# Kernel tuning notes

Hardware: AMD Instinct MI355X
Metric: run time of the kernel (lower is better)

## Reference

```python
import jax, jax.numpy as jnp
import numpy as np

LN_EPS = 1e-5
COS_EPS2 = 1e-16  # torch cosine_similarity: (n1*n2).clamp_min(eps**2), eps=1e-8


def _ln(x, g, b):
    m = jnp.mean(x, -1, keepdims=True)
    v = jnp.mean((x - m) ** 2, -1, keepdims=True)
    return (x - m) * jax.lax.rsqrt(v + LN_EPS) * g + b


def _span_pool(x, starts, ends, word_length):
    # x: [B, S, D] (text_feat[:, 1:]); spans pooled into slots 1..S of a [B, S+1, D] buffer
    B, S, D = x.shape
    cs = jnp.concatenate([jnp.zeros((B, 1, D), x.dtype), jnp.cumsum(x, axis=1)], axis=1)  # [B, S+1, D]
    pool = (jnp.take_along_axis(cs, ends[..., None], axis=1)
            - jnp.take_along_axis(cs, starts[..., None], axis=1))  # [B, S, D]
    mask = (jnp.arange(S)[None, :] < word_length[:, None]).astype(x.dtype)[..., None]
    return jnp.pad(pool * mask, ((0, 0), (1, 0), (0, 0)))  # [B, S+1, D], slot 0 = zeros


def _forward(text_hidden, vit_feature, pooler_out, target_mask, adj,
             ln_g, ln_b, wq, wk, wv, fc_w, mha_ln_g, mha_ln_b,
             w1a, b1a, w1b, b1b, w2a, b2a, w2b, b2b,
             loc_w, loc_b, out_w, out_b, word_length, tran_indices):
    B, L, D = text_hidden.shape
    H = wq.shape[1] // D  # n_head=4, d_k=d_v=768

    # eval mode: all dropouts are identity
    text_feat = _ln(text_hidden, ln_g, ln_b)

    # MultiHeadAttention(text_feat, vit, vit)
    q = (text_feat @ wq).reshape(B, L, H, D)
    k = (vit_feature @ wk).reshape(B, -1, H, D)
    v = (vit_feature @ wv).reshape(B, -1, H, D)
    attn = jnp.einsum('blhd,bmhd->bhlm', q, k) / jnp.sqrt(jnp.asarray(D, text_feat.dtype))
    attn = jax.nn.softmax(attn, axis=-1)
    ctx = jnp.einsum('bhlm,bmhd->blhd', attn, v).reshape(B, L, H * D)
    text_include_img = _ln(ctx @ fc_w + text_feat, mha_ln_g, mha_ln_b)

    # pairwise cosine similarity over sequence positions: [B, L, L]
    n = jnp.linalg.norm(text_include_img, axis=-1)
    sim = jnp.einsum('bld,bmd->blm', text_include_img, text_include_img)
    sim = sim / jnp.maximum(n[:, :, None] * n[:, None, :], COS_EPS2)

    global_bert = _ln(pooler_out, ln_g, ln_b)

    # span pooling of subword features into word slots (tmps buffers)
    starts, ends = tran_indices[..., 0], tran_indices[..., 1]
    tmps = _span_pool(text_feat[:, 1:, :], starts, ends, word_length)
    tmps_ti = _span_pool(text_include_img[:, 1:, :], starts, ends, word_length)

    adj_ti = adj * sim
    den = jnp.sum(adj, axis=2, keepdims=True) + 1.0
    den_ti = jnp.sum(adj_ti, axis=2, keepdims=True) + 1.0

    # NOTE: original loop recomputes from tmps each layer and only keeps the last
    # iteration, so only W1[-1]/W2[-1] affect the output (faithfully reproduced).
    g_dep = jax.nn.relu(((adj @ tmps) @ w1b + b1b) / den)
    g_ti = jax.nn.relu(((adj_ti @ tmps_ti) @ w2b + b2b) / den_ti)

    asp_wn = jnp.sum(target_mask, axis=1, keepdims=True)  # [B, 1]
    m = target_mask[:, :, None]
    gcn_out_text = jnp.sum(g_dep * m, axis=1) / asp_wn
    gcn_out_ti = jnp.sum(g_ti * m, axis=1) / asp_wn

    local_feat = jnp.concatenate([gcn_out_text, gcn_out_ti], axis=1) @ loc_w + loc_b
    feat = jnp.concatenate([global_bert, local_feat], axis=1)
    return feat @ out_w + out_b


def setup_inputs():
    key = jax.random.key(0)
    ks = jax.random.split(key, 20)
    B, L, NV, D, H, NC = 64, 160, 197, 768, 4, 3
    S = L - 1
    s = 0.02
    text_hidden = jax.random.normal(ks[0], (B, L, D), jnp.float32)
    vit_feature = jax.random.normal(ks[1], (B, NV, D), jnp.float32)
    pooler_out = jax.random.normal(ks[2], (B, D), jnp.float32)
    adj = jax.random.uniform(ks[3], (B, L, L), jnp.float32)
    target_mask = jnp.zeros((B, L), jnp.float32).at[:, 1:9].set(1.0)
    word_length = jax.random.randint(ks[4], (B,), 1, S, jnp.int32)
    lens = jax.random.randint(ks[5], (B, S), 1, 3, jnp.int32)  # 1-2 subtokens per word
    cum = jnp.cumsum(lens, axis=1)
    ends = jnp.minimum(cum, S)
    starts = jnp.minimum(cum - lens, S)
    tran_indices = jnp.stack([starts, ends], axis=-1).astype(jnp.int32)
    return dict(
        text_hidden=text_hidden, vit_feature=vit_feature, pooler_out=pooler_out,
        target_mask=target_mask, adj=adj,
        ln_g=jnp.ones((D,), jnp.float32), ln_b=jnp.zeros((D,), jnp.float32),
        wq=jax.random.normal(ks[6], (D, H * D), jnp.float32) * s,
        wk=jax.random.normal(ks[7], (D, H * D), jnp.float32) * s,
        wv=jax.random.normal(ks[8], (D, H * D), jnp.float32) * s,
        fc_w=jax.random.normal(ks[9], (H * D, D), jnp.float32) * s,
        mha_ln_g=jnp.ones((D,), jnp.float32), mha_ln_b=jnp.zeros((D,), jnp.float32),
        w1a=jax.random.normal(ks[10], (D, D), jnp.float32) * s, b1a=jnp.zeros((D,), jnp.float32),
        w1b=jax.random.normal(ks[11], (D, D), jnp.float32) * s, b1b=jnp.zeros((D,), jnp.float32),
        w2a=jax.random.normal(ks[12], (D, D), jnp.float32) * s, b2a=jnp.zeros((D,), jnp.float32),
        w2b=jax.random.normal(ks[13], (D, D), jnp.float32) * s, b2b=jnp.zeros((D,), jnp.float32),
        loc_w=jax.random.normal(ks[14], (2 * D, D), jnp.float32) * s, loc_b=jnp.zeros((D,), jnp.float32),
        out_w=jax.random.normal(ks[15], (2 * D, NC), jnp.float32) * s, out_b=jnp.zeros((NC,), jnp.float32),
        word_length=word_length, tran_indices=tran_indices,
    )


def reference(text_hidden, vit_feature, pooler_out, target_mask, adj,
              ln_g, ln_b, wq, wk, wv, fc_w, mha_ln_g, mha_ln_b,
              w1a, b1a, w1b, b1b, w2a, b2a, w2b, b2b,
              loc_w, loc_b, out_w, out_b, word_length, tran_indices):
    return _forward(text_hidden, vit_feature, pooler_out, target_mask, adj,
                    ln_g, ln_b, wq, wk, wv, fc_w, mha_ln_g, mha_ln_b,
                    w1a, b1a, w1b, b1b, w2a, b2a, w2b, b2b,
                    loc_w, loc_b, out_w, out_b, word_length, tran_indices)
```

## Files before the change

### kernel.cpp

```cpp
#include <hip/hip_runtime.h>
#include <math.h>

#define BB 64
#define LL 160
#define DD 768
#define HH 4
#define NVV 197
#define SS 159

typedef unsigned short u16;
typedef __attribute__((ext_vector_type(8))) short bf16x8;
typedef __attribute__((ext_vector_type(4))) float f32x4;

union QU { uint4 u; bf16x8 v; };

__device__ __forceinline__ u16 f2bf(float a) {
  unsigned u = __builtin_bit_cast(unsigned, a);
  u = (u + 0x7FFFu + ((u >> 16) & 1u)) >> 16;
  return (u16)u;
}
__device__ __forceinline__ unsigned f2bf2(float a, float b) {
  return (unsigned)f2bf(a) | ((unsigned)f2bf(b) << 16);
}
__device__ __forceinline__ float bf2f(u16 h) {
  unsigned u = ((unsigned)h) << 16;
  return __builtin_bit_cast(float, u);
}
__device__ __forceinline__ float to_f(float x) { return x; }
__device__ __forceinline__ float to_f(u16 x) { return bf2f(x); }

__device__ __forceinline__ void async16(const u16* g, void* l) {
  __builtin_amdgcn_global_load_lds(
      (const __attribute__((address_space(1))) void*)g,
      (__attribute__((address_space(3))) void*)l, 16, 0, 0);
}

__device__ __forceinline__ uint4 load_bf8(const u16* __restrict__ P, long long rowbase,
                                          int valid, int kb, int K) {
  uint4 r;
  if (valid && (kb + 8 <= K) && (((rowbase + kb) & 7) == 0)) {
    r = *(const uint4*)(P + rowbase + kb);
  } else {
    u16 e[8];
    #pragma unroll
    for (int i = 0; i < 8; ++i) { int k = kb + i; e[i] = (valid && k < K) ? P[rowbase + k] : (u16)0; }
    r.x = e[0] | ((unsigned)e[1] << 16); r.y = e[2] | ((unsigned)e[3] << 16);
    r.z = e[4] | ((unsigned)e[5] << 16); r.w = e[6] | ((unsigned)e[7] << 16);
  }
  return r;
}

__device__ __forceinline__ uint4 load_row8(const float* __restrict__ P, long long rowbase,
                                           int valid_row, int kb, int K) {
  float f[8];
  if (valid_row && (kb + 8 <= K)) {
    const float4* p0 = (const float4*)(P + rowbase + kb);
    float4 x = p0[0], y = p0[1];
    f[0] = x.x; f[1] = x.y; f[2] = x.z; f[3] = x.w;
    f[4] = y.x; f[5] = y.y; f[6] = y.z; f[7] = y.w;
  } else {
    #pragma unroll
    for (int e = 0; e < 8; ++e) { int k = kb + e; f[e] = (valid_row && k < K) ? P[rowbase + k] : 0.f; }
  }
  uint4 r;
  r.x = f2bf2(f[0], f[1]); r.y = f2bf2(f[2], f[3]);
  r.z = f2bf2(f[4], f[5]); r.w = f2bf2(f[6], f[7]);
  return r;
}

__device__ __forceinline__ uint4 load_a(const u16* P, long long rb, int v, int kb, int K) {
  return load_bf8(P, rb, v, kb, K);
}
__device__ __forceinline__ uint4 load_a(const float* P, long long rb, int v, int kb, int K) {
  return load_row8(P, rb, v, kb, K);
}

__global__ __launch_bounds__(256) void gemm2ph(
    const u16* __restrict__ A, const u16* __restrict__ Bm,
    float* __restrict__ Cf, u16* __restrict__ Cb,
    int M, int N, int K, int lda, int ldb, int ldc, int nbx,
    float alpha, const float* __restrict__ bias, const u16* __restrict__ residB,
    const float* __restrict__ rowdiv, int relu, int accum) {
  __shared__ uint4 As[4][128];
  __shared__ uint4 Bs[4][64];

  int nwg = gridDim.x;
  int id = blockIdx.x;
  int qq = nwg >> 3, rr = nwg & 7;
  int xcd = id & 7, idx = id >> 3;
  int swz = (xcd < rr ? xcd * (qq + 1) : rr * (qq + 1) + (xcd - rr) * qq) + idx;
  int bx = swz % nbx, by = swz / nbx;
  int row0 = by * 128, col0 = bx * 64;

  int t = threadIdx.x, l = t & 63, w = t >> 6;
  int wr = w * 32;
  int nt = K >> 5;

  int ra0 = row0 + l;       if (ra0 > M - 1) ra0 = M - 1;
  int ra1 = row0 + 64 + l;  if (ra1 > M - 1) ra1 = M - 1;
  int rb0 = col0 + l;       if (rb0 > N - 1) rb0 = N - 1;
  const u16* Ap0 = A + (long long)ra0 * lda + w * 8;
  const u16* Ap1 = A + (long long)ra1 * lda + w * 8;
  const u16* Bp0 = Bm + (long long)rb0 * ldb + w * 8;

  f32x4 acc[2][4] = {};

  for (int tt = 0; tt < nt; ++tt) {
    int kk = tt << 5;
    async16(Ap0 + kk, &As[w][0]);
    async16(Ap1 + kk, &As[w][64]);
    async16(Bp0 + kk, &Bs[w][0]);
    __syncthreads();
    int kg = l >> 4, li = l & 15;
    QU a[2], b[4];
    #pragma unroll
    for (int i = 0; i < 2; ++i) a[i].u = As[kg][wr + i * 16 + li];
    #pragma unroll
    for (int j = 0; j < 4; ++j) b[j].u = Bs[kg][j * 16 + li];
    #pragma unroll
    for (int i = 0; i < 2; ++i)
      #pragma unroll
      for (int j = 0; j < 4; ++j)
        acc[i][j] = __builtin_amdgcn_mfma_f32_16x16x32_bf16(a[i].v, b[j].v, acc[i][j], 0, 0, 0);
    __syncthreads();
  }

  #pragma unroll
  for (int i = 0; i < 2; ++i) {
    #pragma unroll
    for (int j = 0; j < 4; ++j) {
      int colj = col0 + j * 16 + (l & 15);
      float bv = (bias && colj < N) ? bias[colj] : 0.f;
      #pragma unroll
      for (int r = 0; r < 4; ++r) {
        int gr = row0 + wr + i * 16 + (l >> 4) * 4 + r;
        if (gr < M && colj < N) {
          long long ci = (long long)gr * ldc + colj;
          float v = acc[i][j][r] * alpha + bv;
          if (residB) v += bf2f(residB[ci]);
          if (accum) v += Cf[ci];
          if (rowdiv) v /= rowdiv[gr];
          if (relu) v = fmaxf(v, 0.f);
          if (Cf) Cf[ci] = v;
          if (Cb) Cb[ci] = f2bf(v);
        }
      }
    }
  }
}

template<bool TRANSB, typename TA>
__global__ __launch_bounds__(256) void gemm_bf16(
    const TA* __restrict__ A, const u16* __restrict__ Bm,
    float* __restrict__ Cf, u16* __restrict__ Cb,
    int M, int N, int K, int lda, int ldb, int ldc, int Hb,
    long long sAb, long long sAh, long long sBb, long long sBh,
    long long sCb, long long sCh,
    float alpha, const float* __restrict__ bias) {
  int bb = blockIdx.z / Hb, hh = blockIdx.z % Hb;
  A += bb * sAb + hh * sAh;
  Bm += bb * sBb + hh * sBh;
  long long coff = bb * sCb + hh * sCh;

  __shared__ uint4 As4[4][64];
  __shared__ uint4 Bs4[4][64];

  int row0 = blockIdx.y * 64, col0 = blockIdx.x * 64;
  int t = threadIdx.x;
  int l = t & 63, w = t >> 6;
  int mq = (w >> 1) * 32, nq = (w & 1) * 32;

  int am = t >> 2, akq = t & 3;
  int bn = t & 63, bkq = t >> 6;

  f32x4 acc[2][2] = {};

  for (int k0 = 0; k0 < K; k0 += 32) {
    As4[akq][am] = load_a(A, (long long)(row0 + am) * lda, (row0 + am) < M, k0 + akq * 8, K);
    if (TRANSB) {
      Bs4[akq][am] = load_bf8(Bm, (long long)(col0 + am) * ldb, (col0 + am) < N, k0 + akq * 8, K);
    } else {
      int gn = col0 + bn;
      u16 e[8];
      #pragma unroll
      for (int i = 0; i < 8; ++i) {
        int k = k0 + bkq * 8 + i;
        e[i] = (gn < N && k < K) ? Bm[(long long)k * ldb + gn] : (u16)0;
      }
      uint4 r;
      r.x = e[0] | ((unsigned)e[1] << 16); r.y = e[2] | ((unsigned)e[3] << 16);
      r.z = e[4] | ((unsigned)e[5] << 16); r.w = e[6] | ((unsigned)e[7] << 16);
      Bs4[bkq][bn] = r;
    }
    __syncthreads();
    int kg = l >> 4, li = l & 15;
    QU a0, a1, b0, b1;
    a0.u = As4[kg][mq + li];
    a1.u = As4[kg][mq + 16 + li];
    b0.u = Bs4[kg][nq + li];
    b1.u = Bs4[kg][nq + 16 + li];
    acc[0][0] = __builtin_amdgcn_mfma_f32_16x16x32_bf16(a0.v, b0.v, acc[0][0], 0, 0, 0);
    acc[0][1] = __builtin_amdgcn_mfma_f32_16x16x32_bf16(a0.v, b1.v, acc[0][1], 0, 0, 0);
    acc[1][0] = __builtin_amdgcn_mfma_f32_16x16x32_bf16(a1.v, b0.v, acc[1][0], 0, 0, 0);
    acc[1][1] = __builtin_amdgcn_mfma_f32_16x16x32_bf16(a1.v, b1.v, acc[1][1], 0, 0, 0);
    __syncthreads();
  }

  #pragma unroll
  for (int i = 0; i < 2; ++i) {
    #pragma unroll
    for (int j = 0; j < 2; ++j) {
      int colj = col0 + nq + j * 16 + (l & 15);
      float bv = (bias && colj < N) ? bias[colj] : 0.f;
      #pragma unroll
      for (int r = 0; r < 4; ++r) {
        int gr = row0 + mq + i * 16 + (l >> 4) * 4 + r;
        if (gr < M && colj < N) {
          long long ci = coff + (long long)gr * ldc + colj;
          float v = acc[i][j][r] * alpha + bv;
          if (Cf) Cf[ci] = v;
          if (Cb) Cb[ci] = f2bf(v);
        }
      }
    }
  }
}

__global__ __launch_bounds__(256) void sim_kernel(
    const float* __restrict__ TII, const float* __restrict__ nrm,
    const float* __restrict__ adjf, u16* __restrict__ adjtiB) {
  int bb = blockIdx.z;
  const float* T = TII + (long long)bb * LL * DD;

  __shared__ uint4 As4[4][64];
  __shared__ uint4 Bs4[4][64];

  int row0 = blockIdx.y * 64, col0 = blockIdx.x * 64;
  int t = threadIdx.x;
  int l = t & 63, w = t >> 6;
  int mq = (w >> 1) * 32, nq = (w & 1) * 32;
  int am = t >> 2, akq = t & 3;

  f32x4 acc[2][2] = {};

  for (int k0 = 0; k0 < DD; k0 += 32) {
    As4[akq][am] = load_row8(T, (long long)(row0 + am) * DD, (row0 + am) < LL, k0 + akq * 8, DD);
    Bs4[akq][am] = load_row8(T, (long long)(col0 + am) * DD, (col0 + am) < LL, k0 + akq * 8, DD);
    __syncthreads();
    int kg = l >> 4, li = l & 15;
    QU a0, a1, b0, b1;
    a0.u = As4[kg][mq + li];
    a1.u = As4[kg][mq + 16 + li];
    b0.u = Bs4[kg][nq + li];
    b1.u = Bs4[kg][nq + 16 + li];
    acc[0][0] = __builtin_amdgcn_mfma_f32_16x16x32_bf16(a0.v, b0.v, acc[0][0], 0, 0, 0);
    acc[0][1] = __builtin_amdgcn_mfma_f32_16x16x32_bf16(a0.v, b1.v, acc[0][1], 0, 0, 0);
    acc[1][0] = __builtin_amdgcn_mfma_f32_16x16x32_bf16(a1.v, b0.v, acc[1][0], 0, 0, 0);
    acc[1][1] = __builtin_amdgcn_mfma_f32_16x16x32_bf16(a1.v, b1.v, acc[1][1], 0, 0, 0);
    __syncthreads();
  }

  #pragma unroll
  for (int i = 0; i < 2; ++i) {
    #pragma unroll
    for (int j = 0; j < 2; ++j) {
      int colj = col0 + nq + j * 16 + (l & 15);
      #pragma unroll
      for (int r = 0; r < 4; ++r) {
        int gr = row0 + mq + i * 16 + (l >> 4) * 4 + r;
        if (gr < LL && colj < LL) {
          float nl = nrm[bb * LL + gr], nm = nrm[bb * LL + colj];
          long long ai = ((long long)bb * LL + gr) * LL + colj;
          float s = acc[i][j][r] / fmaxf(nl * nm, 1e-16f);
          adjtiB[ai] = f2bf(adjf[ai] * s);
        }
      }
    }
  }
}

__device__ __forceinline__ float block_sum(float v, float* sm) {
  #pragma unroll
  for (int o = 32; o > 0; o >>= 1) v += __shfl_down(v, o);
  int lane = threadIdx.x & 63, w = threadIdx.x >> 6;
  if (lane == 0) sm[w] = v;
  __syncthreads();
  if (threadIdx.x == 0) sm[0] = sm[0] + sm[1] + sm[2] + sm[3];
  __syncthreads();
  float r = sm[0];
  __syncthreads();
  return r;
}

__global__ __launch_bounds__(256) void ln_kernel(const float* __restrict__ x, float* __restrict__ yf,
                                                 u16* __restrict__ yb,
                                                 const float* __restrict__ g, const float* __restrict__ b,
                                                 float* __restrict__ nrmout) {
  __shared__ float sm[4];
  long long row = blockIdx.x;
  const float* xr = x + row * DD;
  int t = threadIdx.x;
  float v0 = xr[t], v1 = xr[t + 256], v2 = xr[t + 512];
  float s = block_sum(v0 + v1 + v2, sm);
  float m = s * (1.f / 768.f);
  float d0 = v0 - m, d1 = v1 - m, d2 = v2 - m;
  float vv = block_sum(d0 * d0 + d1 * d1 + d2 * d2, sm);
  float rstd = rsqrtf(vv * (1.f / 768.f) + 1e-5f);
  float y0 = d0 * rstd * g[t] + b[t];
  float y1 = d1 * rstd * g[t + 256] + b[t + 256];
  float y2 = d2 * rstd * g[t + 512] + b[t + 512];
  if (yf) { float* yr = yf + row * DD; yr[t] = y0; yr[t + 256] = y1; yr[t + 512] = y2; }
  if (yb) { u16* yr = yb + row * DD; yr[t] = f2bf(y0); yr[t + 256] = f2bf(y1); yr[t + 512] = f2bf(y2); }
  if (nrmout) {
    float s2 = block_sum(y0 * y0 + y1 * y1 + y2 * y2, sm);
    if (t == 0) nrmout[row] = sqrtf(s2);
  }
}

__global__ __launch_bounds__(256) void softmax_bf16(u16* __restrict__ SP, int nrows) {
  int row = blockIdx.x * 4 + (threadIdx.x >> 6);
  int lane = threadIdx.x & 63;
  if (row >= nrows) return;
  u16* ar = SP + (long long)row * 200;
  float vals[4];
  float mx = -1e30f;
  int cnt = 0;
  for (int i = lane; i < NVV; i += 64) { float v = bf2f(ar[i]); vals[cnt++] = v; mx = fmaxf(mx, v); }
  #pragma unroll
  for (int o = 32; o > 0; o >>= 1) mx = fmaxf(mx, __shfl_xor(mx, o));
  float sum = 0.f;
  for (int j = 0; j < cnt; ++j) { vals[j] = __expf(vals[j] - mx); sum += vals[j]; }
  #pragma unroll
  for (int o = 32; o > 0; o >>= 1) sum += __shfl_xor(sum, o);
  float inv = 1.f / sum;
  cnt = 0;
  for (int i = lane; i < NVV; i += 64) ar[i] = f2bf(vals[cnt++] * inv);
  for (int i = NVV + lane; i < 200; i += 64) ar[i] = 0;
}

template<typename T>
__global__ __launch_bounds__(256) void pool_kernel(const T* __restrict__ src, u16* __restrict__ dst,
                                                   const int* __restrict__ wl, const int* __restrict__ tran) {
  int b = blockIdx.x, i = blockIdx.y, d = threadIdx.x;
  long long ob = ((long long)b * LL + i) * DD;
  float r0 = 0.f, r1 = 0.f, r2 = 0.f;
  if (i > 0 && (i - 1) < wl[b]) {
    int w = i - 1;
    int st = tran[(b * SS + w) * 2];
    int en = tran[(b * SS + w) * 2 + 1];
    const T* sb = src + (long long)b * LL * DD;
    for (int s = st; s < en; ++s) {
      const T* rp = sb + (long long)(1 + s) * DD;
      r0 += to_f(rp[d]); r1 += to_f(rp[d + 256]); r2 += to_f(rp[d + 512]);
    }
  }
  dst[ob + d] = f2bf(r0);
  dst[ob + d + 256] = f2bf(r1);
  dst[ob + d + 512] = f2bf(r2);
}

__global__ __launch_bounds__(256) void den_kernel(const float* __restrict__ adjf, const u16* __restrict__ atB,
                                                  float* __restrict__ den, float* __restrict__ den_ti) {
  __shared__ float sm[4];
  int bl = blockIdx.x, m = threadIdx.x;
  float a = 0.f, at = 0.f;
  if (m < LL) {
    long long idx = (long long)bl * LL + m;
    a = adjf[idx];
    at = bf2f(atB[idx]);
  }
  float sa = block_sum(a, sm);
  float sat = block_sum(at, sm);
  if (m == 0) { den[bl] = sa + 1.f; den_ti[bl] = sat + 1.f; }
}

__global__ __launch_bounds__(256) void gcn_kernel(const u16* __restrict__ g, const float* __restrict__ mask,
                                                  u16* __restrict__ outB, int coloff) {
  int b = blockIdx.x;
  int d = blockIdx.y * 256 + threadIdx.x;
  float s = 0.f, wn = 0.f;
  for (int l = 0; l < LL; ++l) {
    float mk = mask[b * LL + l];
    wn += mk;
    s += mk * bf2f(g[((long long)b * LL + l) * DD + d]);
  }
  outB[(long long)b * (2 * DD) + coloff + d] = f2bf(s / wn);
}

__global__ __launch_bounds__(256) void final_kernel(const float* __restrict__ gb, const float* __restrict__ lf,
                                                    const float* __restrict__ ow, const float* __restrict__ ob,
                                                    float* __restrict__ out) {
  __shared__ float sm[4];
  int b = blockIdx.x / 3, c = blockIdx.x % 3;
  int t = threadIdx.x;
  float s = 0.f;
  for (int k = t; k < DD; k += 256) {
    s += gb[b * DD + k] * ow[k * 3 + c];
    s += lf[b * DD + k] * ow[(DD + k) * 3 + c];
  }
  float tot = block_sum(s, sm);
  if (t == 0) out[b * 3 + c] = tot + ob[c];
}

__global__ __launch_bounds__(256) void conv_kernel(const float4* __restrict__ x, uint2* __restrict__ y, int n4) {
  int i = blockIdx.x * 256 + threadIdx.x;
  if (i < n4) {
    float4 v = x[i];
    uint2 o;
    o.x = f2bf2(v.x, v.y);
    o.y = f2bf2(v.z, v.w);
    y[i] = o;
  }
}

__global__ __launch_bounds__(256) void tconv_kernel(const float* __restrict__ src, u16* __restrict__ dst,
                                                    int R, int C, int lds, int ldd) {
  __shared__ float sm[32][33];
  int t = threadIdx.x;
  int tx = t & 31, ty8 = t >> 5;
  int r0 = blockIdx.y * 32, c0 = blockIdx.x * 32;
  for (int i = ty8; i < 32; i += 8) {
    int r = r0 + i, c = c0 + tx;
    sm[i][tx] = (r < R && c < C) ? src[(long long)r * lds + c] : 0.f;
  }
  __syncthreads();
  for (int i = ty8; i < 32; i += 8) {
    int c = c0 + i, r = r0 + tx;
    if (c < C && r < R) dst[(long long)c * ldd + r] = f2bf(sm[tx][i]);
  }
}

template<typename TA>
static void gemm(hipStream_t s, bool transb, const TA* A, const u16* B, float* Cf, u16* Cb,
                 int M, int N, int K, int lda, int ldb, int ldc, int batches, int Hb,
                 long long sAb, long long sAh, long long sBb, long long sBh,
                 long long sCb, long long sCh, float alpha, const float* bias) {
  dim3 g((N + 63) / 64, (M + 63) / 64, batches);
  if (transb)
    gemm_bf16<true, TA><<<g, 256, 0, s>>>(A, B, Cf, Cb, M, N, K, lda, ldb, ldc, Hb,
                                          sAb, sAh, sBb, sBh, sCb, sCh, alpha, bias);
  else
    gemm_bf16<false, TA><<<g, 256, 0, s>>>(A, B, Cf, Cb, M, N, K, lda, ldb, ldc, Hb,
                                           sAb, sAh, sBb, sBh, sCb, sCh, alpha, bias);
}

static void gemm2phh(hipStream_t s, const u16* A, const u16* B, float* Cf, u16* Cb,
                     int M, int N, int K, int lda, int ldb, int ldc, float alpha,
                     const float* bias, const u16* residB, const float* rowdiv,
                     int relu, int accum) {
  int nbx = (N + 63) / 64, nby = (M + 127) / 128;
  gemm2ph<<<nbx * nby, 256, 0, s>>>(A, B, Cf, Cb, M, N, K, lda, ldb, ldc, nbx,
                                    alpha, bias, residB, rowdiv, relu, accum);
}

extern "C" void kernel_launch(void* const* d_in, const int* in_sizes, int n_in,
                              void* d_out, int out_size, void* d_ws, size_t ws_size,
                              hipStream_t stream) {
  const float* text_hidden = (const float*)d_in[0];
  const float* vit_feature = (const float*)d_in[1];
  const float* pooler_out = (const float*)d_in[2];
  const float* target_mask = (const float*)d_in[3];
  const float* adj = (const float*)d_in[4];
  const float* ln_g = (const float*)d_in[5];
  const float* ln_b = (const float*)d_in[6];
  const float* wq = (const float*)d_in[7];
  const float* wk = (const float*)d_in[8];
  const float* wv = (const float*)d_in[9];
  const float* fc_w = (const float*)d_in[10];
  const float* mha_ln_g = (const float*)d_in[11];
  const float* mha_ln_b = (const float*)d_in[12];
  const float* w1b = (const float*)d_in[15];
  const float* b1b = (const float*)d_in[16];
  const float* w2b = (const float*)d_in[19];
  const float* b2b = (const float*)d_in[20];
  const float* loc_w = (const float*)d_in[21];
  const float* loc_b = (const float*)d_in[22];
  const float* out_w = (const float*)d_in[23];
  const float* out_b = (const float*)d_in[24];
  const int* word_length = (const int*)d_in[25];
  const int* tran = (const int*)d_in[26];
  float* out = (float*)d_out;

  const long long BLD = (long long)BB * LL * DD;
  const long long BND = (long long)BB * NVV * DD;
  const long long WHD = (long long)768 * 768;
  const long long W3K = (long long)768 * 3072;

  char* base = (char*)d_ws;
  auto alloc = [&](size_t bytes) { char* p = base; base += (bytes + 255) & ~(size_t)255; return p; };

  float* R_ACC = (float*)alloc(BLD * 4);
  u16* TFB = (u16*)alloc(BLD * 2);
  u16* vitB = (u16*)alloc(BND * 2);
  u16* BIG = (u16*)alloc((size_t)4 * BLD * 2);
  u16* Mt = (u16*)alloc((size_t)4 * WHD * 2);
  u16* Wvf = (u16*)alloc((size_t)4 * WHD * 2);
  u16* SH = (u16*)alloc((size_t)BB * HH * LL * 200 * 2);
  u16* adjtiB = (u16*)alloc((size_t)BB * LL * LL * 2);
  u16* w1bT = (u16*)alloc(WHD * 2);
  u16* w2bT = (u16*)alloc(WHD * 2);
  u16* locT = (u16*)alloc((size_t)768 * 1536 * 2);
  u16* linB = (u16*)alloc((size_t)BB * 1536 * 2);
  float* nrm = (float*)alloc((size_t)BB * LL * 4);
  float* den = (float*)alloc((size_t)BB * LL * 4);
  float* den_ti = (float*)alloc((size_t)BB * LL * 4);
  float* global_bert = (float*)alloc((size_t)BB * DD * 4);
  float* local_feat = (float*)alloc((size_t)BB * DD * 4);

  u16* wqB = BIG;
  u16* wkB = BIG + W3K;
  u16* wvB = BIG + 2 * W3K;
  u16* fcT = BIG + 3 * W3K;
  u16* T2PV = BIG;
  u16* S4 = SH;
  u16* tmpsTiB = BIG;
  u16* g2B = BIG + BLD;
  u16* H1 = SH;
  u16* tmpsB = vitB;
  u16* h2B = TFB;
  u16* g1B = vitB;

  const float inv_sqrt_d = 1.0f / sqrtf((float)DD);
  const long long sA_L = (long long)LL * DD;

  {
    int n4v = (int)(BND / 4);
    conv_kernel<<<(n4v + 255) / 256, 256, 0, stream>>>((const float4*)vit_feature, (uint2*)vitB, n4v);
    int n4w = (int)(W3K / 4);
    conv_kernel<<<(n4w + 255) / 256, 256, 0, stream>>>((const float4*)wq, (uint2*)wqB, n4w);
    conv_kernel<<<(n4w + 255) / 256, 256, 0, stream>>>((const float4*)wk, (uint2*)wkB, n4w);
    conv_kernel<<<(n4w + 255) / 256, 256, 0, stream>>>((const float4*)wv, (uint2*)wvB, n4w);
    for (int h = 0; h < HH; ++h)
      tconv_kernel<<<dim3(24, 24), 256, 0, stream>>>(fc_w + (size_t)h * WHD, fcT + (size_t)h * WHD,
                                                     768, 768, 768, 768);
    tconv_kernel<<<dim3(24, 24), 256, 0, stream>>>(w1b, w1bT, 768, 768, 768, 768);
    tconv_kernel<<<dim3(24, 24), 256, 0, stream>>>(w2b, w2bT, 768, 768, 768, 768);
    tconv_kernel<<<dim3(24, 48), 256, 0, stream>>>(loc_w, locT, 1536, 768, 768, 1536);
    gemm<u16>(stream, true, wkB, wqB, nullptr, Mt, 768, 768, 768, 3072, 3072, 768,
              HH, 1, 768, 0, 768, 0, WHD, 0, 1.f, nullptr);
    gemm<u16>(stream, true, fcT, wvB, nullptr, Wvf, 768, 768, 768, 768, 3072, 3072,
              HH, 1, WHD, 0, 768, 0, 768, 0, 1.f, nullptr);
  }

  ln_kernel<<<BB * LL, 256, 0, stream>>>(text_hidden, nullptr, TFB, ln_g, ln_b, nullptr);
  gemm2phh(stream, TFB, Mt, nullptr, T2PV, BB * LL, 4 * DD, DD, DD, DD, 4 * DD,
           1.f, nullptr, nullptr, nullptr, 0, 0);
  gemm<u16>(stream, true, T2PV, vitB, nullptr, S4, LL, NVV, DD, 4 * DD, DD, 200,
            BB * HH, HH, (long long)LL * 4 * DD, DD, (long long)NVV * DD, 0,
            (long long)HH * LL * 200, (long long)LL * 200, inv_sqrt_d, nullptr);
  softmax_bf16<<<(BB * HH * LL + 3) / 4, 256, 0, stream>>>(S4, BB * HH * LL);
  gemm<u16>(stream, false, S4, vitB, nullptr, T2PV, LL, DD, NVV, 200, DD, 4 * DD,
            BB * HH, HH, (long long)HH * LL * 200, (long long)LL * 200,
            (long long)NVV * DD, 0, (long long)LL * 4 * DD, DD, 1.f, nullptr);
  gemm2phh(stream, T2PV, Wvf, R_ACC, nullptr, BB * LL, DD, 4 * DD, 4 * DD, 4 * DD, DD,
           1.f, nullptr, TFB, nullptr, 0, 0);

  ln_kernel<<<BB * LL, 256, 0, stream>>>(R_ACC, R_ACC, nullptr, mha_ln_g, mha_ln_b, nrm);
  sim_kernel<<<dim3(3, 3, BB), 256, 0, stream>>>(R_ACC, nrm, adj, adjtiB);
  den_kernel<<<BB * LL, 256, 0, stream>>>(adj, adjtiB, den, den_ti);
  pool_kernel<u16><<<dim3(BB, LL), 256, 0, stream>>>(TFB, tmpsB, word_length, tran);
  pool_kernel<float><<<dim3(BB, LL), 256, 0, stream>>>(R_ACC, tmpsTiB, word_length, tran);
  gemm<float>(stream, false, adj, tmpsB, nullptr, H1, LL, DD, LL, LL, DD, DD,
              BB, 1, (long long)LL * LL, 0, sA_L, 0, sA_L, 0, 1.f, nullptr);
  gemm<u16>(stream, false, adjtiB, tmpsTiB, nullptr, h2B, LL, DD, LL, LL, DD, DD,
            BB, 1, (long long)LL * LL, 0, sA_L, 0, sA_L, 0, 1.f, nullptr);
  gemm2phh(stream, H1, w1bT, nullptr, g1B, BB * LL, DD, DD, DD, DD, DD,
           1.f, b1b, nullptr, den, 1, 0);
  gemm2phh(stream, h2B, w2bT, nullptr, g2B, BB * LL, DD, DD, DD, DD, DD,
           1.f, b2b, nullptr, den_ti, 1, 0);
  gcn_kernel<<<dim3(BB, 3), 256, 0, stream>>>(g1B, target_mask, linB, 0);
  gcn_kernel<<<dim3(BB, 3), 256, 0, stream>>>(g2B, target_mask, linB, DD);
  ln_kernel<<<BB, 256, 0, stream>>>(pooler_out, global_bert, nullptr, ln_g, ln_b, nullptr);
  gemm<u16>(stream, true, linB, locT, local_feat, nullptr, BB, DD, 2 * DD, 2 * DD, 2 * DD, DD,
            1, 1, 0, 0, 0, 0, 0, 0, 1.f, loc_b);
  final_kernel<<<BB * 3, 256, 0, stream>>>(global_bert, local_feat, out_w, out_b, out);
}
```

Before: 843.1 us.

## Replace projection GEMMs with 256-row double-buffered tiles and dual-GEMM launch

Replaces the 128x64 single-buffered projection GEMM with a templated 512-thread kernel that uses 256xBN tiles, a K-step of 64 and double-buffered LDS staging, so loads for the next tile overlap the MFMAs. The two GCN weight GEMMs are merged into one launch through a DUAL mode that splits the grid between two problem sets. It also raises MFMA priority with s_setprio. The larger tiles improve data reuse, but they drop the M and N bounds checks, which assume the dimensions divide evenly, and they increase register and LDS pressure.

```diff
diff --git a/kernel.cpp b/kernel.cpp
--- a/kernel.cpp
+++ b/kernel.cpp
@@ -75,78 +75,128 @@
   return load_row8(P, rb, v, kb, K);
 }
 
-__global__ __launch_bounds__(256) void gemm2ph(
-    const u16* __restrict__ A, const u16* __restrict__ Bm,
-    float* __restrict__ Cf, u16* __restrict__ Cb,
+template<int NREP, int DUAL>
+__global__ __launch_bounds__(512) void gemm_ph(
+    const u16* __restrict__ A0, const u16* __restrict__ B0m,
+    float* __restrict__ Cf0, u16* __restrict__ Cb0,
+    const u16* __restrict__ A1, const u16* __restrict__ B1m,
+    float* __restrict__ Cf1, u16* __restrict__ Cb1,
     int M, int N, int K, int lda, int ldb, int ldc, int nbx,
-    float alpha, const float* __restrict__ bias, const u16* __restrict__ residB,
-    const float* __restrict__ rowdiv, int relu, int accum) {
-  __shared__ uint4 As[4][128];
-  __shared__ uint4 Bs[4][64];
-
-  int nwg = gridDim.x;
+    const float* __restrict__ bias0, const float* __restrict__ bias1,
+    const u16* __restrict__ resid0,
+    const float* __restrict__ rowdiv0, const float* __restrict__ rowdiv1,
+    int relu) {
+  constexpr int BN = NREP * 64;
+  constexpr int BHALF = BN / 2;
+  constexpr int BL = NREP / 2;
+
+  __shared__ uint4 Al[2][2][8][128];
+  __shared__ uint4 Bl[2][2][8][BHALF];
+
   int id = blockIdx.x;
-  int qq = nwg >> 3, rr = nwg & 7;
+  int nset = gridDim.x >> DUAL;
+  int setid = DUAL ? (id >= nset ? 1 : 0) : 0;
+  if (setid) id -= nset;
+  const u16* A = setid ? A1 : A0;
+  const u16* Bm = setid ? B1m : B0m;
+  float* Cf = setid ? Cf1 : Cf0;
+  u16* Cb = setid ? Cb1 : Cb0;
+  const float* bias = setid ? bias1 : bias0;
+  const float* rowdiv = setid ? rowdiv1 : rowdiv0;
+  const u16* residB = setid ? (const u16*)nullptr : resid0;
+
+  int qq = nset >> 3, rr = nset & 7;
   int xcd = id & 7, idx = id >> 3;
   int swz = (xcd < rr ? xcd * (qq + 1) : rr * (qq + 1) + (xcd - rr) * qq) + idx;
   int bx = swz % nbx, by = swz / nbx;
-  int row0 = by * 128, col0 = bx * 64;
+  int row0 = by * 256, col0 = bx * BN;
 
   int t = threadIdx.x, l = t & 63, w = t >> 6;
-  int wr = w * 32;
-  int nt = K >> 5;
-
-  int ra0 = row0 + l;       if (ra0 > M - 1) ra0 = M - 1;
-  int ra1 = row0 + 64 + l;  if (ra1 > M - 1) ra1 = M - 1;
-  int rb0 = col0 + l;       if (rb0 > N - 1) rb0 = N - 1;
-  const u16* Ap0 = A + (long long)ra0 * lda + w * 8;
-  const u16* Ap1 = A + (long long)ra1 * lda + w * 8;
-  const u16* Bp0 = Bm + (long long)rb0 * ldb + w * 8;
-
-  f32x4 acc[2][4] = {};
-
-  for (int tt = 0; tt < nt; ++tt) {
-    int kk = tt << 5;
-    async16(Ap0 + kk, &As[w][0]);
-    async16(Ap1 + kk, &As[w][64]);
-    async16(Bp0 + kk, &Bs[w][0]);
+  int wm = w >> 2, wn = w & 3;
+  int li = l & 15, kg = l >> 4;
+  int nt = K >> 6;
+
+  int aRowL = (w & 1) * 64 + l;
+  int aKs = w >> 1;
+
+  f32x4 acc[8][NREP] = {};
+
+  auto STAGE = [&](int kt, int bi) {
+    long long ko = (long long)kt << 6;
+    const u16* Ab = A + (long long)(row0 + aRowL) * lda + ko + aKs * 8;
+    #pragma unroll
+    for (int ha = 0; ha < 2; ++ha)
+      #pragma unroll
+      for (int i = 0; i < 2; ++i)
+        async16(Ab + (long long)ha * 128 * lda + i * 32, &Al[bi][ha][i * 4 + aKs][(w & 1) * 64]);
+    #pragma unroll
+    for (int hb = 0; hb < 2; ++hb)
+      #pragma unroll
+      for (int i = 0; i < BL; ++i) {
+        int s0 = i * 512 + w * 64;
+        int bks = s0 / BHALF;
+        int br0 = s0 % BHALF;
+        async16(Bm + (long long)(col0 + hb * BHALF + br0 + l) * ldb + ko + bks * 8,
+                &Bl[bi][hb][bks][br0]);
+      }
+  };
+
+  STAGE(0, 0);
+  __syncthreads();
+
+  int buf = 0;
+  for (int kt = 0; kt < nt; ++kt) {
+    if (kt + 1 < nt) STAGE(kt + 1, buf ^ 1);
+    QU bF[NREP][2];
+    #pragma unroll
+    for (int n = 0; n < NREP; ++n) {
+      int colp = wn * (16 * NREP) + n * 16 + li;
+      int hb = colp / BHALF, rb = colp % BHALF;
+      #pragma unroll
+      for (int s32 = 0; s32 < 2; ++s32)
+        bF[n][s32].u = Bl[buf][hb][s32 * 4 + kg][rb];
+    }
+    #pragma unroll
+    for (int mh = 0; mh < 2; ++mh) {
+      QU aF[4][2];
+      #pragma unroll
+      for (int m = 0; m < 4; ++m)
+        #pragma unroll
+        for (int s32 = 0; s32 < 2; ++s32)
+          aF[m][s32].u = Al[buf][wm][s32 * 4 + kg][(mh * 4 + m) * 16 + li];
+      __builtin_amdgcn_s_setprio(1);
+      #pragma unroll
+      for (int m = 0; m < 4; ++m)
+        #pragma unroll
+        for (int n = 0; n < NREP; ++n)
+          #pragma unroll
+          for (int s32 = 0; s32 < 2; ++s32)
+            acc[mh * 4 + m][n] = __builtin_amdgcn_mfma_f32_16x16x32_bf16(
+                aF[m][s32].v, bF[n][s32].v, acc[mh * 4 + m][n], 0, 0, 0);
+      __builtin_amdgcn_s_setprio(0);
+    }
     __syncthreads();
-    int kg = l >> 4, li = l & 15;
-    QU a[2], b[4];
-    #pragma unroll
-    for (int i = 0; i < 2; ++i) a[i].u = As[kg][wr + i * 16 + li];
-    #pragma unroll
-    for (int j = 0; j < 4; ++j) b[j].u = Bs[kg][j * 16 + li];
-    #pragma unroll
-    for (int i = 0; i < 2; ++i)
-      #pragma unroll
-      for (int j = 0; j < 4; ++j)
-        acc[i][j] = __builtin_amdgcn_mfma_f32_16x16x32_bf16(a[i].v, b[j].v, acc[i][j], 0, 0, 0);
-    __syncthreads();
+    buf ^= 1;
   }
 
   #pragma unroll
-  for (int i = 0; i < 2; ++i) {
-    #pragma unroll
-    for (int j = 0; j < 4; ++j) {
-      int colj = col0 + j * 16 + (l & 15);
-      float bv = (bias && colj < N) ? bias[colj] : 0.f;
+  for (int m = 0; m < 8; ++m)
+    #pragma unroll
+    for (int n = 0; n < NREP; ++n) {
+      int col = col0 + wn * (16 * NREP) + n * 16 + li;
+      float bv = bias ? bias[col] : 0.f;
       #pragma unroll
       for (int r = 0; r < 4; ++r) {
-        int gr = row0 + wr + i * 16 + (l >> 4) * 4 + r;
-        if (gr < M && colj < N) {
-          long long ci = (long long)gr * ldc + colj;
-          float v = acc[i][j][r] * alpha + bv;
-          if (residB) v += bf2f(residB[ci]);
-          if (accum) v += Cf[ci];
-          if (rowdiv) v /= rowdiv[gr];
-          if (relu) v = fmaxf(v, 0.f);
-          if (Cf) Cf[ci] = v;
-          if (Cb) Cb[ci] = f2bf(v);
-        }
+        int row = row0 + wm * 128 + m * 16 + kg * 4 + r;
+        long long ci = (long long)row * ldc + col;
+        float v = acc[m][n][r] + bv;
+        if (residB) v += bf2f(residB[ci]);
+        if (rowdiv) v /= rowdiv[row];
+        if (relu) v = fmaxf(v, 0.f);
+        if (Cf) Cf[ci] = v;
+        if (Cb) Cb[ci] = f2bf(v);
       }
     }
-  }
 }
 
 template<bool TRANSB, typename TA>
@@ -442,15 +492,6 @@
   else
     gemm_bf16<false, TA><<<g, 256, 0, s>>>(A, B, Cf, Cb, M, N, K, lda, ldb, ldc, Hb,
                                            sAb, sAh, sBb, sBh, sCb, sCh, alpha, bias);
-}
-
-static void gemm2phh(hipStream_t s, const u16* A, const u16* B, float* Cf, u16* Cb,
-                     int M, int N, int K, int lda, int ldb, int ldc, float alpha,
-                     const float* bias, const u16* residB, const float* rowdiv,
-                     int relu, int accum) {
-  int nbx = (N + 63) / 64, nby = (M + 127) / 128;
-  gemm2ph<<<nbx * nby, 256, 0, s>>>(A, B, Cf, Cb, M, N, K, lda, ldb, ldc, nbx,
-                                    alpha, bias, residB, rowdiv, relu, accum);
 }
 
 extern "C" void kernel_launch(void* const* d_in, const int* in_sizes, int n_in,
@@ -543,8 +584,10 @@
   }
 
   ln_kernel<<<BB * LL, 256, 0, stream>>>(text_hidden, nullptr, TFB, ln_g, ln_b, nullptr);
-  gemm2phh(stream, TFB, Mt, nullptr, T2PV, BB * LL, 4 * DD, DD, DD, DD, 4 * DD,
-           1.f, nullptr, nullptr, nullptr, 0, 0);
+  gemm_ph<4, 0><<<480, 512, 0, stream>>>(TFB, Mt, nullptr, T2PV,
+                                         nullptr, nullptr, nullptr, nullptr,
+                                         BB * LL, 4 * DD, DD, DD, DD, 4 * DD, 12,
+                                         nullptr, nullptr, nullptr, nullptr, nullptr, 0);
   gemm<u16>(stream, true, T2PV, vitB, nullptr, S4, LL, NVV, DD, 4 * DD, DD, 200,
             BB * HH, HH, (long long)LL * 4 * DD, DD, (long long)NVV * DD, 0,
             (long long)HH * LL * 200, (long long)LL * 200, inv_sqrt_d, nullptr);
@@ -552,8 +595,10 @@
   gemm<u16>(stream, false, S4, vitB, nullptr, T2PV, LL, DD, NVV, 200, DD, 4 * DD,
             BB * HH, HH, (long long)HH * LL * 200, (long long)LL * 200,
             (long long)NVV * DD, 0, (long long)LL * 4 * DD, DD, 1.f, nullptr);
-  gemm2phh(stream, T2PV, Wvf, R_ACC, nullptr, BB * LL, DD, 4 * DD, 4 * DD, 4 * DD, DD,
-           1.f, nullptr, TFB, nullptr, 0, 0);
+  gemm_ph<2, 0><<<240, 512, 0, stream>>>(T2PV, Wvf, R_ACC, nullptr,
+                                         nullptr, nullptr, nullptr, nullptr,
+                                         BB * LL, DD, 4 * DD, 4 * DD, 4 * DD, DD, 6,
+                                         nullptr, nullptr, TFB, nullptr, nullptr, 0);
 
   ln_kernel<<<BB * LL, 256, 0, stream>>>(R_ACC, R_ACC, nullptr, mha_ln_g, mha_ln_b, nrm);
   sim_kernel<<<dim3(3, 3, BB), 256, 0, stream>>>(R_ACC, nrm, adj, adjtiB);
@@ -564,10 +609,10 @@
               BB, 1, (long long)LL * LL, 0, sA_L, 0, sA_L, 0, 1.f, nullptr);
   gemm<u16>(stream, false, adjtiB, tmpsTiB, nullptr, h2B, LL, DD, LL, LL, DD, DD,
             BB, 1, (long long)LL * LL, 0, sA_L, 0, sA_L, 0, 1.f, nullptr);
-  gemm2phh(stream, H1, w1bT, nullptr, g1B, BB * LL, DD, DD, DD, DD, DD,
-           1.f, b1b, nullptr, den, 1, 0);
-  gemm2phh(stream, h2B, w2bT, nullptr, g2B, BB * LL, DD, DD, DD, DD, DD,
-           1.f, b2b, nullptr, den_ti, 1, 0);
+  gemm_ph<4, 1><<<240, 512, 0, stream>>>(H1, w1bT, nullptr, g1B,
+                                         h2B, w2bT, nullptr, g2B,
+                                         BB * LL, DD, DD, DD, DD, DD, 3,
+                                         b1b, b2b, nullptr, den, den_ti, 1);
   gcn_kernel<<<dim3(BB, 3), 256, 0, stream>>>(g1B, target_mask, linB, 0);
   gcn_kernel<<<dim3(BB, 3), 256, 0, stream>>>(g2B, target_mask, linB, DD);
   ln_kernel<<<BB, 256, 0, stream>>>(pooler_out, global_bert, nullptr, ln_g, ln_b, nullptr);
```

New measurement: 737.0 us. 12.6% less time.
